# Kernel tuning notes

Hardware: AMD Instinct MI355X
Metric: run time of the kernel (lower is better)

The kernel has to match this reference:

```python
import jax, jax.numpy as jnp
import numpy as np

DIM = 128
EDGE_COUNT = 128
N_NODES = 128
GRAPH_COUNT = 8
VOCAB = 100000
VEC_DIM = 300


def setup_inputs():
    key = jax.random.key(0)
    ks = jax.random.split(key, 8)
    rng = np.random.default_rng(0)
    data = jnp.asarray(rng.integers(0, VOCAB, size=N_NODES), dtype=jnp.int32)
    types = jnp.zeros((N_NODES,), dtype=jnp.int32)  # single data_type
    edges = jnp.asarray(rng.integers(0, EDGE_COUNT, size=N_NODES), dtype=jnp.int32)
    # parent-offset trees: node i's parent is a node > i, last node is the single root (offset 0)
    g = np.zeros((GRAPH_COUNT, N_NODES), dtype=np.int32)
    for j in range(GRAPH_COUNT):
        for i in range(N_NODES - 1):
            p = int(rng.integers(i + 1, N_NODES))
            g[j, i] = p - i
    graphs = jnp.asarray(g)
    inv_sqrt_d = 1.0 / np.sqrt(DIM)
    inv_sqrt_v = 1.0 / np.sqrt(VEC_DIM)
    return {
        "data": data, "types": types, "graphs": graphs, "edges": edges, "pos": 37,
        "data_vecs": jax.random.normal(ks[0], (VOCAB, VEC_DIM), jnp.float32),
        "data_weights": jax.random.normal(ks[1], (VEC_DIM, DIM), jnp.float32) * inv_sqrt_v,
        "data_biases": jax.random.normal(ks[2], (DIM,), jnp.float32) * 0.1,
        "edge_weights": jax.random.normal(ks[3], (EDGE_COUNT, DIM, DIM), jnp.float32) * inv_sqrt_d,
        "edge_biases": jax.random.normal(ks[4], (EDGE_COUNT, DIM), jnp.float32) * 0.1,
        "score_embedding_weights": jax.random.normal(ks[5], (DIM, 1), jnp.float32) * inv_sqrt_d,
        "score_data_weights": jax.random.normal(ks[6], (DIM, 1), jnp.float32) * inv_sqrt_d,
        "score_bias": jax.random.normal(ks[7], (1, 1), jnp.float32),
    }


def _tree_structure(parents_row):
    # Faithful reproduction of calc_embedding's structure handling (numpy on int constants).
    parents = np.asarray(parents_row).copy()
    n = len(parents)
    roots = [i for i in range(n) if parents[i] == 0]
    for i in range(len(roots) - 1):
        parents[roots[i]] = roots[i + 1]
    root = roots[-1]
    parents[root] = -n
    children = {}
    for i in range(n):
        pp = i + int(parents[i])
        children.setdefault(pp, []).append(i)
    order = []  # DFS preorder from root; reversed gives children-before-parent
    stack = [root]
    while stack:
        node = stack.pop()
        order.append(node)
        stack.extend(children.get(node, []))
    return root, children, order


def _forward(data, types, graphs, edges, pos,
             data_vecs, data_weights, data_biases,
             edge_weights, edge_biases,
             score_embedding_weights, score_data_weights, score_bias):
    data_np = np.asarray(data)
    graphs_np = np.asarray(graphs)
    edges_np = np.asarray(edges).copy()
    E, D, _ = edge_weights.shape
    # data embedding + data score for the queried position
    d_emb = data_vecs[data_np[pos]] @ data_weights + data_biases          # (D,)
    d_score = score_bias[0, 0] + d_emb @ score_data_weights[:, 0]         # scalar
    edges_np[pos] = -1  # unknown edge at pos -> branch over all edge types
    # base embeddings for all nodes at once: (N, D)
    base = data_vecs[data_np] @ data_weights + data_biases

    def transform(child_emb, eid):
        # child_emb: (E, D). eid < 0 -> per-edge-type weights (baddbmm over all E edges)
        if eid < 0:
            return jnp.einsum('ed,edk->ek', child_emb, edge_weights) + edge_biases
        return child_emb @ edge_weights[eid] + edge_biases[eid]

    scores = []
    for j in range(graphs_np.shape[0]):
        root, children, order = _tree_structure(graphs_np[j])
        emb = {}
        for n in reversed(order):  # children before parents
            e = jnp.broadcast_to(base[n], (E, D))
            ch = children.get(n, [])
            for c in ch:
                e = e + transform(emb.pop(c), int(edges_np[c]))
            if ch:
                e = jax.nn.relu(e)  # clamp(min=0) only for internal nodes
            emb[n] = e
        res = transform(emb[root], int(edges_np[root]))  # add_child_embedding(zeros, root_emb, edges[root])
        scores.append(d_score + res @ score_embedding_weights[:, 0])  # (E,)
    return jnp.stack(scores)  # (GRAPH_COUNT, EDGE_COUNT)


def reference(data, types, graphs, edges, pos, data_vecs, data_weights, data_biases,
              edge_weights, edge_biases, score_embedding_weights, score_data_weights, score_bias):
    return _forward(data, types, graphs, edges, pos, data_vecs, data_weights, data_biases,
                    edge_weights, edge_biases, score_embedding_weights, score_data_weights, score_bias)
```

## Files before the change

kernel.cpp:

```cpp
#include <hip/hip_runtime.h>
#include <stdint.h>


#define NND 128
#define DD  128
#define GG  8
#define VD  300
#define EDGEN 128
#define CH2 16
#define KSP 8

typedef unsigned int u32;

#define F_POS  (1<<16)
#define F_PATH (1<<17)
#define SKIPF  (F_POS|F_PATH)

__global__ void __launch_bounds__(128) k_base(
        const int* __restrict__ data, const int* __restrict__ posArr,
        const float* __restrict__ vecs, const float* __restrict__ dw,
        const float* __restrict__ db,   const float* __restrict__ sdw,
        const float* __restrict__ sb,
        float* __restrict__ base, float* __restrict__ dscore,
        int* __restrict__ flagsG)
{
    __shared__ __align__(16) float row[VD];
    __shared__ float red[DD];
    int n = blockIdx.x, t = threadIdx.x;
    if (n < GG) flagsG[n*NND + t] = 0;
    int id = data[n];
    const float4* vp = (const float4*)(vecs + (size_t)id * VD);
    for (int i = t; i < VD/4; i += 128) ((float4*)row)[i] = vp[i];
    __syncthreads();
    float a0 = db[t], a1 = 0.f, a2 = 0.f, a3 = 0.f;
    for (int d = 0; d < VD; d += 4){
        a0 = fmaf(row[d+0], dw[(d+0)*DD + t], a0);
        a1 = fmaf(row[d+1], dw[(d+1)*DD + t], a1);
        a2 = fmaf(row[d+2], dw[(d+2)*DD + t], a2);
        a3 = fmaf(row[d+3], dw[(d+3)*DD + t], a3);
    }
    float acc = (a0 + a1) + (a2 + a3);
    base[n*DD + t] = acc;
    if (n == posArr[0]){
        red[t] = acc * sdw[t];
        __syncthreads();
        for (int o = 64; o > 0; o >>= 1){ if (t < o) red[t] += red[t+o]; __syncthreads(); }
        if (t == 0) dscore[0] = sb[0] + red[0];
    }
}

__global__ void __launch_bounds__(1024, 1) k_treeX(
        const int* __restrict__ graphs, const int* __restrict__ edges,
        const int* __restrict__ posArr, const float* __restrict__ EW,
        const float* __restrict__ EB,   const float* __restrict__ base,
        float* __restrict__ vposG, float* __restrict__ uG, int* __restrict__ meta,
        float* __restrict__ contribX, int* __restrict__ flagsG)
{
    __shared__ __align__(16) float xstage[16][DD];
    __shared__ int par_s[NND], eid_s[NND], flg_s[NND];
    __shared__ int ccnt[NND], cstart[NND], cidx[NND];
    __shared__ int dep[NND], anc[NND], lcnt[NND], lstart[NND], order[NND];
    __shared__ int maxD_s;

    int b = blockIdx.x, g = b >> 3, k = b & (KSP-1), t = threadIdx.x;

    if (t < NND){
        par_s[t] = (t < NND-1) ? (t + graphs[g*NND + t]) : (NND-1);
        eid_s[t] = edges[t];
        flg_s[t] = 0;
        ccnt[t]  = 0;
        lcnt[t]  = 0;
    }
    if (t == 0) maxD_s = 0;
    __syncthreads();

    int mySlot = 0;
    if (t < NND-1){
        int p = par_s[t];
        atomicAdd(&ccnt[p], 1);
        for (int c = 0; c < t; ++c) mySlot += (par_s[c] == p);
    }
    if (t < NND){
        dep[t] = (t < NND-1) ? 1 : 0;
        anc[t] = par_s[t];
    }
    if (t == 0){
        int p = posArr[0];
        flg_s[p] |= F_POS;
        int c = par_s[p], s = 0;
        for (;;){
            flg_s[c] |= F_PATH | (s << 24);
            if (k == 0) meta[g*(NND+1) + 1 + s] = c;
            ++s;
            if (c == NND-1) break;
            c = par_s[c];
        }
        if (k == 0) meta[g*(NND+1)] = s;
    }
    __syncthreads();

    if (t < NND){
        int s = 0;
        for (int p = 0; p < t; ++p) s += ccnt[p];
        cstart[t] = s;
    }
    __syncthreads();
    if (t < NND-1) cidx[cstart[par_s[t]] + mySlot] = t;

    for (int kk = 0; kk < 7; ++kk){
        int d2 = 0, a2 = 0;
        if (t < NND){ d2 = dep[t] + dep[anc[t]]; a2 = anc[anc[t]]; }
        __syncthreads();
        if (t < NND){ dep[t] = d2; anc[t] = a2; }
        __syncthreads();
    }
    if (t < NND) atomicMax(&maxD_s, dep[t]);
    if (t < NND) atomicAdd(&lcnt[dep[t]], 1);
    __syncthreads();

    if (t < NND){
        int s = 0;
        for (int d2 = 0; d2 < t; ++d2) s += lcnt[d2];
        lstart[t] = s;
    }
    __syncthreads();
    if (t < NND){
        int d2 = dep[t], s = 0;
        for (int c = 0; c < t; ++c) s += (dep[c] == d2);
        order[lstart[d2] + s] = t;
    }
    __syncthreads();

    int w = t >> 6, l = t & 63;
    int c0 = 2*l;
    int li = l & 31, hl = l >> 5;
    int c4 = 4*li, dbase = 64*hl;
    int maxD = maxD_s;

    for (int d = maxD; d >= 0; --d){
        int lo = lstart[d], cnt = lcnt[d];
        for (int q = k + KSP*w; q < cnt; q += KSP*16){
            int n = order[lo + q];
            float2 bse = *(const float2*)&base[n*DD + c0];
            float e0 = bse.x, e1 = bse.y;
            int cs = cstart[n], cc = ccnt[n];
            for (int j0 = 0; j0 < cc; j0 += 4){
                float2 v0, v1, v2, v3;
                int u0=0, u1=0, u2=0, u3=0;
                if (j0+0 < cc){ int c = cidx[cs+j0+0];
                    if (!(flg_s[c] & SKIPF)){ v0 = *(const float2*)&contribX[((size_t)g*NND+c)*DD + c0]; u0=1; } }
                if (j0+1 < cc){ int c = cidx[cs+j0+1];
                    if (!(flg_s[c] & SKIPF)){ v1 = *(const float2*)&contribX[((size_t)g*NND+c)*DD + c0]; u1=1; } }
                if (j0+2 < cc){ int c = cidx[cs+j0+2];
                    if (!(flg_s[c] & SKIPF)){ v2 = *(const float2*)&contribX[((size_t)g*NND+c)*DD + c0]; u2=1; } }
                if (j0+3 < cc){ int c = cidx[cs+j0+3];
                    if (!(flg_s[c] & SKIPF)){ v3 = *(const float2*)&contribX[((size_t)g*NND+c)*DD + c0]; u3=1; } }
                if (u0){ e0 += v0.x; e1 += v0.y; }
                if (u1){ e0 += v1.x; e1 += v1.y; }
                if (u2){ e0 += v2.x; e1 += v2.y; }
                if (u3){ e0 += v3.x; e1 += v3.y; }
            }
            int f = flg_s[n];
            if (f & F_POS){
                if (cc){ e0 = fmaxf(e0, 0.f); e1 = fmaxf(e1, 0.f); }
                *(float2*)&vposG[g*DD + c0] = make_float2(e0, e1);
            } else if (f & F_PATH){
                int slot = ((u32)f) >> 24;
                *(float2*)&uG[((size_t)g*NND + slot)*DD + c0] = make_float2(e0, e1);
            } else {
                if (cc){ e0 = fmaxf(e0, 0.f); e1 = fmaxf(e1, 0.f); }
                *(float2*)&xstage[w][c0] = make_float2(e0, e1);
                asm volatile("s_waitcnt lgkmcnt(0)" ::: "memory");
                int e = eid_s[n];
                const float* Wp = EW + (size_t)e*(DD*DD) + (size_t)dbase*DD + c4;
                const float* xr = &xstage[w][dbase];
                float4 A[8], B[8];
                float s0=0.f, s1=0.f, s2=0.f, s3=0.f;
                #define LW(buf, gi) { _Pragma("unroll") \
                    for (int j2 = 0; j2 < 8; ++j2) \
                        buf[j2] = *(const float4*)&Wp[(size_t)((gi)*8 + j2)*DD]; }
                #define CP(buf, gi) { _Pragma("unroll") \
                    for (int j2 = 0; j2 < 8; ++j2){ \
                        float x = xr[(gi)*8 + j2]; \
                        s0 = fmaf(x, buf[j2].x, s0); s1 = fmaf(x, buf[j2].y, s1); \
                        s2 = fmaf(x, buf[j2].z, s2); s3 = fmaf(x, buf[j2].w, s3); } }
                LW(A,0); LW(B,1);
                CP(A,0); LW(A,2);
                CP(B,1); LW(B,3);
                CP(A,2); LW(A,4);
                CP(B,3); LW(B,5);
                CP(A,4); LW(A,6);
                CP(B,5); LW(B,7);
                CP(A,6);
                CP(B,7);
                #undef LW
                #undef CP
                s0 += __shfl_xor(s0, 32); s1 += __shfl_xor(s1, 32);
                s2 += __shfl_xor(s2, 32); s3 += __shfl_xor(s3, 32);
                if (hl == 0){
                    float4 bb = *(const float4*)&EB[(size_t)e*DD + c4];
                    *(float4*)&contribX[((size_t)g*NND + n)*DD + c4] =
                        make_float4(s0 + bb.x, s1 + bb.y, s2 + bb.z, s3 + bb.w);
                }
            }
        }
        __syncthreads();
        if (d > 0){
            if (t == 0){
                __threadfence();
                atomicAdd(&flagsG[g*NND + d], 1);
                while (__hip_atomic_load(&flagsG[g*NND + d],
                        __ATOMIC_ACQUIRE, __HIP_MEMORY_SCOPE_AGENT) < KSP)
                    __builtin_amdgcn_s_sleep(1);
                __threadfence();
            }
            __syncthreads();
        }
    }
}

__global__ void __launch_bounds__(256, 1) k_step0(
        const float* __restrict__ EW, const float* __restrict__ EB,
        const float* __restrict__ vposG, const float* __restrict__ uG,
        float* __restrict__ V0)
{
    __shared__ __align__(16) float vpos_s[GG][DD];
    int e = blockIdx.x, t = threadIdx.x, l = t & 63, w = t >> 6;
    {
        int idx = t;
        ((float4*)vpos_s)[idx] = ((const float4*)vposG)[idx];
    }
    __syncthreads();
    int k4 = w*8 + (l & 7);
    int d0 = (l >> 3) * 16;
    bool owner = ((l >> 3) == 0);
    const float* Wp = EW + (size_t)e*(DD*DD) + (size_t)d0*DD + 4*k4;
    float4 wr[16];
    #pragma unroll
    for (int d = 0; d < 16; ++d) wr[d] = *(const float4*)&Wp[d*DD];
    float4 bb = *(const float4*)&EB[(size_t)e*DD + 4*k4];
    for (int g = 0; g < GG; ++g){
        float s0=0.f, s1=0.f, s2=0.f, s3=0.f;
        #pragma unroll
        for (int d = 0; d < 16; ++d){
            float x = vpos_s[g][d0 + d];
            s0 = fmaf(x, wr[d].x, s0);
            s1 = fmaf(x, wr[d].y, s1);
            s2 = fmaf(x, wr[d].z, s2);
            s3 = fmaf(x, wr[d].w, s3);
        }
        #pragma unroll
        for (int m = 8; m <= 32; m <<= 1){
            s0 += __shfl_xor(s0, m); s1 += __shfl_xor(s1, m);
            s2 += __shfl_xor(s2, m); s3 += __shfl_xor(s3, m);
        }
        if (owner){
            float4 u0 = *(const float4*)&uG[(size_t)g*NND*DD + 4*k4];
            float4 r;
            r.x = fmaxf(u0.x + s0 + bb.x, 0.f);
            r.y = fmaxf(u0.y + s1 + bb.y, 0.f);
            r.z = fmaxf(u0.z + s2 + bb.z, 0.f);
            r.w = fmaxf(u0.w + s3 + bb.w, 0.f);
            *(float4*)&V0[((size_t)g*EDGEN + e)*DD + 4*k4] = r;
        }
    }
}

__global__ void __launch_bounds__(256, 1) k_steps(
        const int* __restrict__ edges,
        const float* __restrict__ EW, const float* __restrict__ EB,
        const float* __restrict__ SEW,
        const float* __restrict__ uG, const float* __restrict__ V0,
        const int* __restrict__ meta, const float* __restrict__ dscore,
        float* __restrict__ outp)
{
    __shared__ __align__(16) float Vbuf[2][CH2][DD];
    __shared__ float red[CH2][4];
    int g = blockIdx.x >> 3, chunk = blockIdx.x & 7;
    int t = threadIdx.x, l = t & 63, w = t >> 6;
    int k4 = w*8 + (l & 7);
    int d0 = (l >> 3) * 16;
    bool owner = ((l >> 3) == 0);
    int eBase = chunk * CH2;
    int L = meta[g*(NND+1)];

    for (int idx = t; idx < CH2*DD/4; idx += 256)
        ((float4*)&Vbuf[0][0][0])[idx] =
            ((const float4*)&V0[((size_t)g*EDGEN + eBase)*DD])[idx];
    __syncthreads();

    int cur = 0;
    for (int s = 1; s < L; ++s){
        int pn = meta[g*(NND+1) + s];
        int ej = edges[pn];
        const float* Wp = EW + (size_t)ej*(DD*DD) + (size_t)d0*DD + 4*k4;
        float4 wr[16];
        #pragma unroll
        for (int d = 0; d < 16; ++d) wr[d] = *(const float4*)&Wp[d*DD];
        float4 us = *(const float4*)&uG[((size_t)g*NND + s)*DD + 4*k4];
        float4 bb = *(const float4*)&EB[(size_t)ej*DD + 4*k4];
        #pragma unroll 4
        for (int p = 0; p < CH2; ++p){
            float ev[16];
            #pragma unroll
            for (int j = 0; j < 4; ++j){
                float4 x = *(const float4*)&Vbuf[cur][p][d0 + 4*j];
                ev[4*j+0]=x.x; ev[4*j+1]=x.y; ev[4*j+2]=x.z; ev[4*j+3]=x.w;
            }
            float s0=0.f, s1=0.f, s2=0.f, s3=0.f;
            #pragma unroll
            for (int d = 0; d < 16; ++d){
                s0 = fmaf(ev[d], wr[d].x, s0);
                s1 = fmaf(ev[d], wr[d].y, s1);
                s2 = fmaf(ev[d], wr[d].z, s2);
                s3 = fmaf(ev[d], wr[d].w, s3);
            }
            #pragma unroll
            for (int m = 8; m <= 32; m <<= 1){
                s0 += __shfl_xor(s0, m); s1 += __shfl_xor(s1, m);
                s2 += __shfl_xor(s2, m); s3 += __shfl_xor(s3, m);
            }
            if (owner){
                float4 r;
                r.x = fmaxf(us.x + s0 + bb.x, 0.f);
                r.y = fmaxf(us.y + s1 + bb.y, 0.f);
                r.z = fmaxf(us.z + s2 + bb.z, 0.f);
                r.w = fmaxf(us.w + s3 + bb.w, 0.f);
                *(float4*)&Vbuf[cur^1][p][4*k4] = r;
            }
        }
        __syncthreads();
        cur ^= 1;
    }

    {
        int rn = meta[g*(NND+1) + L];
        int er = edges[rn];
        const float* Wp = EW + (size_t)er*(DD*DD) + (size_t)d0*DD + 4*k4;
        float4 wr[16];
        #pragma unroll
        for (int d = 0; d < 16; ++d) wr[d] = *(const float4*)&Wp[d*DD];
        float4 bb = *(const float4*)&EB[(size_t)er*DD + 4*k4];
        float4 sw = *(const float4*)&SEW[4*k4];
        #pragma unroll 4
        for (int p = 0; p < CH2; ++p){
            float ev[16];
            #pragma unroll
            for (int j = 0; j < 4; ++j){
                float4 x = *(const float4*)&Vbuf[cur][p][d0 + 4*j];
                ev[4*j+0]=x.x; ev[4*j+1]=x.y; ev[4*j+2]=x.z; ev[4*j+3]=x.w;
            }
            float s0=0.f, s1=0.f, s2=0.f, s3=0.f;
            #pragma unroll
            for (int d = 0; d < 16; ++d){
                s0 = fmaf(ev[d], wr[d].x, s0);
                s1 = fmaf(ev[d], wr[d].y, s1);
                s2 = fmaf(ev[d], wr[d].z, s2);
                s3 = fmaf(ev[d], wr[d].w, s3);
            }
            #pragma unroll
            for (int m = 8; m <= 32; m <<= 1){
                s0 += __shfl_xor(s0, m); s1 += __shfl_xor(s1, m);
                s2 += __shfl_xor(s2, m); s3 += __shfl_xor(s3, m);
            }
            if (owner){
                float part = (s0 + bb.x) * sw.x + (s1 + bb.y) * sw.y
                           + (s2 + bb.z) * sw.z + (s3 + bb.w) * sw.w;
                part += __shfl_xor(part, 1);
                part += __shfl_xor(part, 2);
                part += __shfl_xor(part, 4);
                if (l == 0) red[p][w] = part;
            }
        }
        __syncthreads();
        if (t < CH2)
            outp[g*DD + eBase + t] = dscore[0] + red[t][0] + red[t][1] + red[t][2] + red[t][3];
    }
}

extern "C" void kernel_launch(void* const* d_in, const int* in_sizes, int n_in,
                              void* d_out, int out_size, void* d_ws, size_t ws_size,
                              hipStream_t stream)
{
    const int*   data   = (const int*)d_in[0];
    const int*   graphs = (const int*)d_in[2];
    const int*   edges  = (const int*)d_in[3];
    const int*   posArr = (const int*)d_in[4];
    const float* vecs   = (const float*)d_in[5];
    const float* dw     = (const float*)d_in[6];
    const float* db     = (const float*)d_in[7];
    const float* ew     = (const float*)d_in[8];
    const float* eb     = (const float*)d_in[9];
    const float* sew    = (const float*)d_in[10];
    const float* sdw    = (const float*)d_in[11];
    const float* sb     = (const float*)d_in[12];

    char* ws = (char*)d_ws;
    float* base   = (float*)(ws);
    float* vposG  = (float*)(ws + 65536);
    float* uG     = (float*)(ws + 69632);
    float* dscore = (float*)(ws + 593920);
    int*   meta   = (int*)  (ws + 594176);
    float* V0     = (float*)(ws + 598528);
    float* contribX = V0;
    int*   flagsG = (int*)  (ws + 1122816);

    float* outp = (float*)d_out;

    k_base <<<NND, 128, 0, stream>>>(data, posArr, vecs, dw, db, sdw, sb,
                                     base, dscore, flagsG);
    k_treeX<<<GG*KSP, 1024, 0, stream>>>(graphs, edges, posArr, ew, eb, base,
                                         vposG, uG, meta, contribX, flagsG);
    k_step0<<<EDGEN, 256, 0, stream>>>(ew, eb, vposG, uG, V0);
    k_steps<<<GG*(EDGEN/CH2), 256, 0, stream>>>(edges, ew, eb, sew, uG, V0,
                                                meta, dscore, outp);
}
```

Measured before the change: 318.5 us.

## Halve treeX block size and deepen weight-load pipeline with inline asm

Shrinks the tree kernel from 1024 to 512 threads per block, with 8 staging rows instead of 16 and a matching node stride. The 64-row edge-weight matvec now uses hand-written global_load_dwordx4 batches. Five groups of eight float4 loads are kept in flight, controlled by explicit vmcnt waits and sched barriers. The aim is to hide global-memory latency on the serial per-level critical path with more loads in flight per wave. In exchange, each block has fewer waves per level, register pressure rises, and the fragile asm waits could break correctness if the counts are wrong.

```diff
diff --git a/kernel.cpp b/kernel.cpp
--- a/kernel.cpp
+++ b/kernel.cpp
@@ -49,14 +49,14 @@
     }
 }
 
-__global__ void __launch_bounds__(1024, 1) k_treeX(
+__global__ void __launch_bounds__(512, 1) k_treeX(
         const int* __restrict__ graphs, const int* __restrict__ edges,
         const int* __restrict__ posArr, const float* __restrict__ EW,
         const float* __restrict__ EB,   const float* __restrict__ base,
         float* __restrict__ vposG, float* __restrict__ uG, int* __restrict__ meta,
         float* __restrict__ contribX, int* __restrict__ flagsG)
 {
-    __shared__ __align__(16) float xstage[16][DD];
+    __shared__ __align__(16) float xstage[8][DD];
     __shared__ int par_s[NND], eid_s[NND], flg_s[NND];
     __shared__ int ccnt[NND], cstart[NND], cidx[NND];
     __shared__ int dep[NND], anc[NND], lcnt[NND], lstart[NND], order[NND];
@@ -139,7 +139,7 @@
 
     for (int d = maxD; d >= 0; --d){
         int lo = lstart[d], cnt = lcnt[d];
-        for (int q = k + KSP*w; q < cnt; q += KSP*16){
+        for (int q = k + KSP*w; q < cnt; q += KSP*8){
             int n = order[lo + q];
             float2 bse = *(const float2*)&base[n*DD + c0];
             float e0 = bse.x, e1 = bse.y;
@@ -174,27 +174,55 @@
                 int e = eid_s[n];
                 const float* Wp = EW + (size_t)e*(DD*DD) + (size_t)dbase*DD + c4;
                 const float* xr = &xstage[w][dbase];
-                float4 A[8], B[8];
                 float s0=0.f, s1=0.f, s2=0.f, s3=0.f;
-                #define LW(buf, gi) { _Pragma("unroll") \
-                    for (int j2 = 0; j2 < 8; ++j2) \
-                        buf[j2] = *(const float4*)&Wp[(size_t)((gi)*8 + j2)*DD]; }
-                #define CP(buf, gi) { _Pragma("unroll") \
-                    for (int j2 = 0; j2 < 8; ++j2){ \
-                        float x = xr[(gi)*8 + j2]; \
-                        s0 = fmaf(x, buf[j2].x, s0); s1 = fmaf(x, buf[j2].y, s1); \
-                        s2 = fmaf(x, buf[j2].z, s2); s3 = fmaf(x, buf[j2].w, s3); } }
-                LW(A,0); LW(B,1);
-                CP(A,0); LW(A,2);
-                CP(B,1); LW(B,3);
-                CP(A,2); LW(A,4);
-                CP(B,3); LW(B,5);
-                CP(A,4); LW(A,6);
-                CP(B,5); LW(B,7);
-                CP(A,6);
-                CP(B,7);
-                #undef LW
-                #undef CP
+                float4 Pa0,Pa1,Pa2,Pa3,Pa4,Pa5,Pa6,Pa7;
+                float4 Pb0,Pb1,Pb2,Pb3,Pb4,Pb5,Pb6,Pb7;
+                float4 Pc0,Pc1,Pc2,Pc3,Pc4,Pc5,Pc6,Pc7;
+                float4 Pd0,Pd1,Pd2,Pd3,Pd4,Pd5,Pd6,Pd7;
+                float4 Pe0,Pe1,Pe2,Pe3,Pe4,Pe5,Pe6,Pe7;
+#define GISS(B, pp) \
+    asm volatile("global_load_dwordx4 %0, %8, off\n\t" \
+                 "global_load_dwordx4 %1, %8, off offset:512\n\t" \
+                 "global_load_dwordx4 %2, %8, off offset:1024\n\t" \
+                 "global_load_dwordx4 %3, %8, off offset:1536\n\t" \
+                 "global_load_dwordx4 %4, %8, off offset:2048\n\t" \
+                 "global_load_dwordx4 %5, %8, off offset:2560\n\t" \
+                 "global_load_dwordx4 %6, %8, off offset:3072\n\t" \
+                 "global_load_dwordx4 %7, %8, off offset:3584" \
+                 : "=&v"(B##0),"=&v"(B##1),"=&v"(B##2),"=&v"(B##3), \
+                   "=&v"(B##4),"=&v"(B##5),"=&v"(B##6),"=&v"(B##7) : "v"(pp))
+#define GW(n) do { asm volatile("s_waitcnt vmcnt(" #n ")" ::: "memory"); \
+                   __builtin_amdgcn_sched_barrier(0); } while(0)
+#define GCONS(B, kk) do { \
+    float4 xa = *(const float4*)&xr[(kk)*8]; \
+    float4 xb = *(const float4*)&xr[(kk)*8 + 4]; \
+    s0=fmaf(xa.x,(B##0).x,s0); s1=fmaf(xa.x,(B##0).y,s1); s2=fmaf(xa.x,(B##0).z,s2); s3=fmaf(xa.x,(B##0).w,s3); \
+    s0=fmaf(xa.y,(B##1).x,s0); s1=fmaf(xa.y,(B##1).y,s1); s2=fmaf(xa.y,(B##1).z,s2); s3=fmaf(xa.y,(B##1).w,s3); \
+    s0=fmaf(xa.z,(B##2).x,s0); s1=fmaf(xa.z,(B##2).y,s1); s2=fmaf(xa.z,(B##2).z,s2); s3=fmaf(xa.z,(B##2).w,s3); \
+    s0=fmaf(xa.w,(B##3).x,s0); s1=fmaf(xa.w,(B##3).y,s1); s2=fmaf(xa.w,(B##3).z,s2); s3=fmaf(xa.w,(B##3).w,s3); \
+    s0=fmaf(xb.x,(B##4).x,s0); s1=fmaf(xb.x,(B##4).y,s1); s2=fmaf(xb.x,(B##4).z,s2); s3=fmaf(xb.x,(B##4).w,s3); \
+    s0=fmaf(xb.y,(B##5).x,s0); s1=fmaf(xb.y,(B##5).y,s1); s2=fmaf(xb.y,(B##5).z,s2); s3=fmaf(xb.y,(B##5).w,s3); \
+    s0=fmaf(xb.z,(B##6).x,s0); s1=fmaf(xb.z,(B##6).y,s1); s2=fmaf(xb.z,(B##6).z,s2); s3=fmaf(xb.z,(B##6).w,s3); \
+    s0=fmaf(xb.w,(B##7).x,s0); s1=fmaf(xb.w,(B##7).y,s1); s2=fmaf(xb.w,(B##7).z,s2); s3=fmaf(xb.w,(B##7).w,s3); \
+    } while(0)
+                asm volatile("s_waitcnt vmcnt(0)" ::: "memory");
+                __builtin_amdgcn_sched_barrier(0);
+                GISS(Pa, Wp);
+                GISS(Pb, Wp + 1024);
+                GISS(Pc, Wp + 2048);
+                GISS(Pd, Wp + 3072);
+                GISS(Pe, Wp + 4096);
+                GW(32); GCONS(Pa, 0); GISS(Pa, Wp + 5120);
+                GW(32); GCONS(Pb, 1); GISS(Pb, Wp + 6144);
+                GW(32); GCONS(Pc, 2); GISS(Pc, Wp + 7168);
+                GW(24); GCONS(Pd, 3);
+                GW(16); GCONS(Pe, 4);
+                GW(8);  GCONS(Pa, 5);
+                GW(4);  GCONS(Pb, 6);
+                GW(0);  GCONS(Pc, 7);
+#undef GISS
+#undef GW
+#undef GCONS
                 s0 += __shfl_xor(s0, 32); s1 += __shfl_xor(s1, 32);
                 s2 += __shfl_xor(s2, 32); s3 += __shfl_xor(s3, 32);
                 if (hl == 0){
@@ -409,8 +437,8 @@
 
     k_base <<<NND, 128, 0, stream>>>(data, posArr, vecs, dw, db, sdw, sb,
                                      base, dscore, flagsG);
-    k_treeX<<<GG*KSP, 1024, 0, stream>>>(graphs, edges, posArr, ew, eb, base,
-                                         vposG, uG, meta, contribX, flagsG);
+    k_treeX<<<GG*KSP, 512, 0, stream>>>(graphs, edges, posArr, ew, eb, base,
+                                        vposG, uG, meta, contribX, flagsG);
     k_step0<<<EDGEN, 256, 0, stream>>>(ew, eb, vposG, uG, V0);
     k_steps<<<GG*(EDGEN/CH2), 256, 0, stream>>>(edges, ew, eb, sew, uG, V0,
                                                 meta, dscore, outp);
```

New measurement: 318.4 us. No clear change (-0.1%).
